# Kernel tuning notes

Hardware: AMD Instinct MI355X
Metric: run time of the kernel (lower is better)

The kernel has to match this reference:

```python
import jax, jax.numpy as jnp
import numpy as np

NB_ATOMS = 1024
NB_CHANNELS = 3
ATOM_SIZE = 16
NONDIFF_STEPS = 30
DIFF_STEPS = 10
TEMP = 100.0
EPS = 1e-8
BATCH = 16384


def setup_inputs() -> dict:
    key = jax.random.key(0)
    k1, k2 = jax.random.split(key)
    y = jax.random.normal(k1, (BATCH, NB_CHANNELS, ATOM_SIZE, ATOM_SIZE), dtype=jnp.float32)
    # init='random': randn / (atom_size * sqrt(nb_channels))
    atoms = jax.random.normal(k2, (NB_ATOMS, NB_CHANNELS, ATOM_SIZE, ATOM_SIZE), dtype=jnp.float32)
    atoms = atoms / (ATOM_SIZE * np.sqrt(NB_CHANNELS).astype(np.float32))
    return {"y": y, "atoms": atoms}


def reference(y, atoms):
    B = y.shape[0]
    A = atoms.shape[0]
    # L1 norms per sample / per atom
    y_norms = jnp.sum(jnp.abs(y.reshape(B, -1)), axis=1).reshape(-1, 1, 1, 1)  # [B,1,1,1]
    a_flat = atoms.reshape(A, -1)
    a_flat = a_flat / jnp.sum(jnp.abs(a_flat), axis=1, keepdims=True)          # [A,D]

    X = a_flat @ a_flat.T                                   # [A,A] gram matrix
    q = a_flat @ (y / y_norms).reshape(B, -1).T             # [A,B]
    coeffs = jnp.full((A, B), 1.0 / A, dtype=y.dtype)

    Xs = jax.lax.stop_gradient(X)
    qs = jax.lax.stop_gradient(q)

    def nondiff_step(i, c):
        grad = Xs @ c - qs                                  # [A,B]
        # faithful to torch: argmin over the BATCH dim, scatter one 1 per atom row
        am = jnp.zeros_like(c).at[jnp.arange(A), jnp.argmin(grad, axis=1)].set(1.0)
        d = am - c
        denom = jnp.sum(d * (Xs @ d)) + EPS                 # scalar (as in torch)
        lam = jnp.clip(-jnp.sum(d * grad, axis=0)[None, :] / denom, 0.0, 1.0)
        return c + d * lam

    coeffs = jax.lax.fori_loop(0, NONDIFF_STEPS, nondiff_step, coeffs)
    coeffs = jax.lax.stop_gradient(coeffs)

    def diff_step(c, _):
        grad = X @ c - q
        sm = jax.nn.softmax(-TEMP * grad, axis=0)           # softmax over atoms
        d = sm - c
        denom = jnp.sum(d * (X @ d)) + EPS
        lam = jnp.clip(-jnp.sum(d * grad, axis=0)[None, :] / denom, 0.0, 1.0)
        return c + d * lam, None

    coeffs, _ = jax.lax.scan(diff_step, coeffs, None, length=DIFF_STEPS)

    # einsum 'ij,ilmn->jlmn' with normalized atoms, rescale by y L1 norms
    recon = (coeffs.T @ a_flat).reshape(B, NB_CHANNELS, ATOM_SIZE, ATOM_SIZE) * y_norms
    return recon
```

## Files before the change

kernel.cpp:

```cpp
#include <hip/hip_runtime.h>
#include <hip/hip_bf16.h>
#include <math.h>

#define A_DIM 1024
#define D_DIM 768
#define B_DIM 16384
#define TEMP_C 100.0f
#define EPS_C 1e-8f


typedef __attribute__((ext_vector_type(8))) short short8;
typedef __attribute__((ext_vector_type(4))) float f32x4;
#define MFMA16(a, b, c) __builtin_amdgcn_mfma_f32_16x16x32_bf16(a, b, c, 0, 0, 0)

typedef __attribute__((address_space(3))) unsigned char lds_byte;
typedef __attribute__((address_space(1))) const unsigned char g_byte;
__device__ __forceinline__ void async_copy16(const void* gptr, void* lptr) {
    __builtin_amdgcn_global_load_lds((g_byte*)gptr, (lds_byte*)lptr, 16, 0, 0);
}

#define SCHED0 __builtin_amdgcn_sched_barrier(0)
#define ASM_BAR asm volatile("s_barrier" ::: "memory")

__device__ __forceinline__ void swz(int i, int& m0, int& n0) {
    int xcd = i & 7, j = i >> 3;
    m0 = ((xcd << 4) + (j >> 3)) << 7;
    n0 = (j & 7) << 7;
}


__device__ __forceinline__ float wave_sum(float v) {
#pragma unroll
    for (int m = 1; m < 64; m <<= 1) v += __shfl_xor(v, m);
    return v;
}
__device__ __forceinline__ float wave_max(float v) {
#pragma unroll
    for (int m = 1; m < 64; m <<= 1) v = fmaxf(v, __shfl_xor(v, m));
    return v;
}

__device__ __forceinline__ float block_reduce_sum(float v, float* red) {
    int t = threadIdx.x;
    v = wave_sum(v);
    if ((t & 63) == 0) red[t >> 6] = v;
    __syncthreads();
    float r = red[0] + red[1] + red[2] + red[3];
    __syncthreads();
    return r;
}

__device__ __forceinline__ float block_reduce_max(float v, float* red) {
    int t = threadIdx.x;
    v = wave_max(v);
    if ((t & 63) == 0) red[t >> 6] = v;
    __syncthreads();
    float r = fmaxf(fmaxf(red[0], red[1]), fmaxf(red[2], red[3]));
    __syncthreads();
    return r;
}

__device__ __forceinline__ void block_reduce_sum3(float& a, float& b, float& c, float* red) {
    int t = threadIdx.x;
    a = wave_sum(a);
    b = wave_sum(b);
    c = wave_sum(c);
    if ((t & 63) == 0) {
        int w = t >> 6;
        red[w] = a; red[4 + w] = b; red[8 + w] = c;
    }
    __syncthreads();
    a = red[0] + red[1] + red[2] + red[3];
    b = red[4] + red[5] + red[6] + red[7];
    c = red[8] + red[9] + red[10] + red[11];
    __syncthreads();
}


__device__ __forceinline__ unsigned int fkey(float v) {
    unsigned int u = __float_as_uint(v);
    return u ^ ((u & 0x80000000u) ? 0xFFFFFFFFu : 0x80000000u);
}

__device__ __forceinline__ unsigned short f2bf(float x) {
    unsigned int u = __float_as_uint(x);
    return (unsigned short)((u + 0x7FFFu + ((u >> 16) & 1u)) >> 16);
}
__device__ __forceinline__ float bf2f(unsigned short h) {
    return __uint_as_float(((unsigned int)h) << 16);
}
__device__ __forceinline__ void split2(float x, unsigned short& hi, unsigned short& lo) {
    hi = f2bf(x);
    lo = f2bf(x - bf2f(hi));
}
__device__ __forceinline__ float clamp01(float x) {
    return fminf(fmaxf(x, 0.f), 1.f);
}


__device__ __forceinline__ void stage_tile8(const unsigned short* gsrc, int stride, int k0,
                                            unsigned short* ltile, int lane) {
    int srow = lane >> 2;
    int scol = (lane & 3) * 8;
#pragma unroll
    for (int s = 0; s < 8; s++) {
        const unsigned short* src = gsrc + (size_t)(s * 16 + srow) * stride + k0 + scol;
        async_copy16(src, ltile + s * 512);
    }
}

__device__ __forceinline__ void mfma_k32(const unsigned short* lds, int wm, int wn, int lane,
                                         f32x4 acc[4][4]) {
    int frow = lane & 15, fk = (lane >> 4) * 8;
    short8 ah[4], al[4], bh[4], bl[4];
#pragma unroll
    for (int t = 0; t < 4; t++) {
        int ar = (wm * 64 + t * 16 + frow) * 32 + fk;
        ah[t] = *(const short8*)&lds[ar];
        al[t] = *(const short8*)&lds[4096 + ar];
        int br = (wn * 64 + t * 16 + frow) * 32 + fk;
        bh[t] = *(const short8*)&lds[8192 + br];
        bl[t] = *(const short8*)&lds[12288 + br];
    }
#pragma unroll
    for (int i = 0; i < 4; i++)
#pragma unroll
        for (int j = 0; j < 4; j++) {
            acc[i][j] = MFMA16(ah[i], bh[j], acc[i][j]);
            acc[i][j] = MFMA16(ah[i], bl[j], acc[i][j]);
            acc[i][j] = MFMA16(al[i], bh[j], acc[i][j]);
        }
}


template <int PART>
__device__ __forceinline__ void stage_part(unsigned short* buf,
                                           const unsigned short* Ahi,
                                           const unsigned short* Alo,
                                           const unsigned short* Xhi,
                                           const unsigned short* Xlo,
                                           int m0, int n0, int k0, int t) {
    constexpr int AHI = 0;
    constexpr int ALO = 8192;
    constexpr int BHI = 16384;
    constexpr int BLO = 24576;
    int r = t >> 2;
    int cg = (t & 3) ^ ((t >> 3) & 3);
    size_t col = (size_t)k0 + cg * 8;
    if constexpr (PART == 0) {
        async_copy16(Ahi + (size_t)(m0 + r) * A_DIM + col,       buf + AHI + t * 8);
        async_copy16(Ahi + (size_t)(m0 + 128 + r) * A_DIM + col, buf + AHI + 4096 + t * 8);
    } else if constexpr (PART == 1) {
        async_copy16(Alo + (size_t)(m0 + r) * A_DIM + col,       buf + ALO + t * 8);
        async_copy16(Alo + (size_t)(m0 + 128 + r) * A_DIM + col, buf + ALO + 4096 + t * 8);
    } else if constexpr (PART == 2) {
        async_copy16(Xhi + (size_t)(n0 + r) * A_DIM + col,       buf + BHI + t * 8);
        async_copy16(Xhi + (size_t)(n0 + 128 + r) * A_DIM + col, buf + BHI + 4096 + t * 8);
    } else {
        async_copy16(Xlo + (size_t)(n0 + r) * A_DIM + col,       buf + BLO + t * 8);
        async_copy16(Xlo + (size_t)(n0 + 128 + r) * A_DIM + col, buf + BLO + 4096 + t * 8);
    }
}

__device__ __forceinline__ void mfma_mi3(short8 ah, short8 al,
                                         const short8 bh[4], const short8 bl[4],
                                         f32x4* accRow) {
#pragma unroll
    for (int j = 0; j < 4; j++) {
        accRow[j] = MFMA16(ah, bh[j], accRow[j]);
        accRow[j] = MFMA16(ah, bl[j], accRow[j]);
        accRow[j] = MFMA16(al, bh[j], accRow[j]);
    }
}

template <int MODE>
__global__ __launch_bounds__(512, 2) void gemm256(const unsigned short* __restrict__ Ahi,
                                                  const unsigned short* __restrict__ Alo,
                                                  const unsigned short* __restrict__ Xhi,
                                                  const unsigned short* __restrict__ Xlo,
                                                  const float* __restrict__ qt,
                                                  unsigned long long* __restrict__ keys,
                                                  float* __restrict__ cxc,
                                                  float* __restrict__ cq,
                                                  float* __restrict__ scal,
                                                  float* __restrict__ G,
                                                  float* __restrict__ scal3,
                                                  float* __restrict__ XC) {
    constexpr int BUFS = 32768;
    constexpr int AHI = 0;
    constexpr int ALO = 8192;
    constexpr int BHI = 16384;
    constexpr int BLO = 24576;
    __shared__ unsigned short lds[2 * BUFS];
    __shared__ float red[8];
    int tid = threadIdx.x;
    if (MODE == 0 && blockIdx.x == 0 && tid < 4) scal[tid] = 0.f;
    int w = tid >> 6, lane = tid & 63;
    int wm = w >> 2, wn = w & 3;
    int bi = blockIdx.x;
    int xcd = bi & 7, bj = bi >> 3;
    int m0 = ((xcd << 3) + (bj >> 2)) << 8;
    int n0 = (bj & 3) << 8;

    f32x4 acc[8][4];
#pragma unroll
    for (int i = 0; i < 8; i++)
#pragma unroll
        for (int j = 0; j < 4; j++) acc[i][j] = f32x4{0.f, 0.f, 0.f, 0.f};

    int frow = lane & 15;
    int sw = ((lane >> 4) ^ ((frow >> 1) & 3)) * 8;

    stage_part<0>(lds, Ahi, Alo, Xhi, Xlo, m0, n0, 0, tid);
    stage_part<1>(lds, Ahi, Alo, Xhi, Xlo, m0, n0, 0, tid);
    stage_part<2>(lds, Ahi, Alo, Xhi, Xlo, m0, n0, 0, tid);
    stage_part<3>(lds, Ahi, Alo, Xhi, Xlo, m0, n0, 0, tid);

    int cur = 0;
    for (int ks = 0; ks < 32; ++ks) {
        unsigned short* rb = lds + cur * BUFS;
        unsigned short* wb = lds + (cur ^ 1) * BUFS;
        const bool pf = (ks < 31);
        const int k1 = (ks + 1) * 32;

        if (pf) {
            stage_part<0>(wb, Ahi, Alo, Xhi, Xlo, m0, n0, k1, tid);
            SCHED0;
            asm volatile("s_waitcnt vmcnt(2)" ::: "memory");
        } else {
            asm volatile("s_waitcnt vmcnt(0)" ::: "memory");
        }
        SCHED0; ASM_BAR; SCHED0;

        short8 bh[4], bl[4];
#pragma unroll
        for (int j = 0; j < 4; j++) {
            int br = wn * 64 + j * 16 + frow;
            bh[j] = *(const short8*)&rb[BHI + br * 32 + sw];
            bl[j] = *(const short8*)&rb[BLO + br * 32 + sw];
        }
        {
            int ar0 = wm * 128 + 0 * 16 + frow, ar1 = wm * 128 + 1 * 16 + frow;
            short8 a0h = *(const short8*)&rb[AHI + ar0 * 32 + sw];
            short8 a1h = *(const short8*)&rb[AHI + ar1 * 32 + sw];
            short8 a0l = *(const short8*)&rb[ALO + ar0 * 32 + sw];
            short8 a1l = *(const short8*)&rb[ALO + ar1 * 32 + sw];
            if (pf) stage_part<1>(wb, Ahi, Alo, Xhi, Xlo, m0, n0, k1, tid);
            SCHED0; ASM_BAR; SCHED0;
            asm volatile("s_waitcnt lgkmcnt(0)" ::: "memory"); SCHED0;
            __builtin_amdgcn_s_setprio(1);
            mfma_mi3(a0h, a0l, bh, bl, acc[0]);
            mfma_mi3(a1h, a1l, bh, bl, acc[1]);
            __builtin_amdgcn_s_setprio(0);
            SCHED0; ASM_BAR; SCHED0;
        }
#pragma unroll
        for (int ph = 1; ph < 4; ph++) {
            int mia = 2 * ph, mib = 2 * ph + 1;
            int ara = wm * 128 + mia * 16 + frow, arb = wm * 128 + mib * 16 + frow;
            short8 aah = *(const short8*)&rb[AHI + ara * 32 + sw];
            short8 abh = *(const short8*)&rb[AHI + arb * 32 + sw];
            short8 aal = *(const short8*)&rb[ALO + ara * 32 + sw];
            short8 abl = *(const short8*)&rb[ALO + arb * 32 + sw];
            if (pf) {
                if (ph == 1) stage_part<2>(wb, Ahi, Alo, Xhi, Xlo, m0, n0, k1, tid);
                if (ph == 2) stage_part<3>(wb, Ahi, Alo, Xhi, Xlo, m0, n0, k1, tid);
            }
            SCHED0; ASM_BAR; SCHED0;
            asm volatile("s_waitcnt lgkmcnt(0)" ::: "memory"); SCHED0;
            __builtin_amdgcn_s_setprio(1);
            mfma_mi3(aah, aal, bh, bl, acc[mia]);
            mfma_mi3(abh, abl, bh, bl, acc[mib]);
            __builtin_amdgcn_s_setprio(0);
            SCHED0; ASM_BAR; SCHED0;
        }
        cur ^= 1;
    }

    int crow = (lane >> 4) * 4, ccol = lane & 15;
    if constexpr (MODE == 0) {
        unsigned long long best[4] = {~0ULL, ~0ULL, ~0ULL, ~0ULL};
#pragma unroll
        for (int mi = 0; mi < 8; mi++)
#pragma unroll
            for (int r = 0; r < 4; r++) {
                int gm = m0 + wm * 128 + mi * 16 + crow + r;
                float pcx = 0.f, pcq = 0.f;
#pragma unroll
                for (int jj = 0; jj < 4; jj++) {
                    int gn = n0 + wn * 64 + jj * 16 + ccol;
                    size_t idx = (size_t)gm * A_DIM + gn;
                    float c = bf2f(Ahi[idx]) + bf2f(Alo[idx]);
                    float q = qt[idx];
                    float xc = acc[mi][jj][r];
                    XC[idx] = xc;
                    pcx += c * xc;
                    pcq += c * q;
                    unsigned long long key =
                        ((unsigned long long)fkey(xc - q) << 32) | (unsigned int)gm;
                    if (key < best[jj]) best[jj] = key;
                }
                for (int mm = 1; mm < 16; mm <<= 1) {
                    pcx += __shfl_xor(pcx, mm, 16);
                    pcq += __shfl_xor(pcq, mm, 16);
                }
                if (ccol == 0) {
                    atomicAdd(&cxc[gm], pcx);
                    atomicAdd(&cq[gm], pcq);
                }
            }
#pragma unroll
        for (int jj = 0; jj < 4; jj++) {
            int gn = n0 + wn * 64 + jj * 16 + ccol;
            unsigned long long o = __shfl_xor(best[jj], 16);
            if (o < best[jj]) best[jj] = o;
            o = __shfl_xor(best[jj], 32);
            if (o < best[jj]) best[jj] = o;
            if ((lane >> 4) == 0) atomicMin(&keys[gn], best[jj]);
        }
    } else {
        float part = 0.f;
#pragma unroll
        for (int mi = 0; mi < 8; mi++)
#pragma unroll
            for (int r = 0; r < 4; r++) {
                int gm = m0 + wm * 128 + mi * 16 + crow + r;
#pragma unroll
                for (int jj = 0; jj < 4; jj++) {
                    int gn = n0 + wn * 64 + jj * 16 + ccol;
                    size_t idx = (size_t)gm * A_DIM + gn;
                    float d = bf2f(Ahi[idx]) + bf2f(Alo[idx]);
                    float xd = acc[mi][jj][r];
                    G[idx] = xd;
                    part += xd * d;
                }
            }
        part = wave_sum(part);
        if (lane == 0) red[w] = part;
        __syncthreads();
        if (tid == 0) {
            float tot = red[0] + red[1] + red[2] + red[3] +
                        red[4] + red[5] + red[6] + red[7];
            atomicAdd(scal3, tot);
        }
    }
}

__global__ __launch_bounds__(512) void fgrad(const float* __restrict__ qt,
                                             unsigned short* __restrict__ Chi,
                                             unsigned short* __restrict__ Clo,
                                             float* __restrict__ XC,
                                             const float* __restrict__ Xf,
                                             const unsigned long long* __restrict__ Kprev,
                                             unsigned long long* __restrict__ Kcur,
                                             float* __restrict__ cxc,
                                             float* __restrict__ cq,
                                             float* __restrict__ num_amg,
                                             const float* __restrict__ scalPrev,
                                             float* __restrict__ scalCur) {
    __shared__ unsigned long long lkeys[8][1024];
    int tid = threadIdx.x;
    if (blockIdx.x == 0 && tid < 4) scalCur[tid] = 0.f;
    int w = tid >> 6, lane = tid & 63;
    int b0 = blockIdx.x * 32;
    float den = scalPrev[0] + scalPrev[1] - 2.f * scalPrev[2] + EPS_C;

    unsigned int klow[16];
#pragma unroll
    for (int s = 0; s < 16; s++) klow[s] = (unsigned int)Kprev[lane + s * 64];

    unsigned long long best[16];
#pragma unroll
    for (int i = 0; i < 16; i++) best[i] = ~0ULL;

    for (int rr = 0; rr < 4; ++rr) {
        int b = b0 + w + rr * 8;
        float lam = clamp01((cxc[b] - cq[b] - num_amg[b]) / den);
        float om = 1.f - lam;
        const bool active = (lam != 0.f);

        unsigned short* hr = Chi + (size_t)b * A_DIM;
        unsigned short* lr = Clo + (size_t)b * A_DIM;
        float* xcr = XC + (size_t)b * A_DIM;
        const float* qr = qt + (size_t)b * A_DIM;
        float dx = 0.f, dq = 0.f;

        if (active) {
            unsigned long long mask[16];
#pragma unroll
            for (int s = 0; s < 16; s++) mask[s] = __ballot(klow[s] == (unsigned int)b);
#pragma unroll
            for (int ch = 0; ch < 4; ++ch) {
                int col = ch * 256 + lane * 4;
                ushort4 hv = *(const ushort4*)(hr + col);
                ushort4 lv = *(const ushort4*)(lr + col);
                float4 xv = *(const float4*)(xcr + col);
                float4 qv = *(const float4*)(qr + col);
                int sel = lane >> 4;
                unsigned long long mw =
                    (sel == 0) ? mask[ch * 4 + 0] :
                    (sel == 1) ? mask[ch * 4 + 1] :
                    (sel == 2) ? mask[ch * 4 + 2] : mask[ch * 4 + 3];
                unsigned int ind4 = (unsigned int)((mw >> ((lane & 15) * 4)) & 0xFULL);
                float c0 = om * (bf2f(hv.x) + bf2f(lv.x)) + ((ind4 & 1u) ? lam : 0.f);
                float c1 = om * (bf2f(hv.y) + bf2f(lv.y)) + ((ind4 & 2u) ? lam : 0.f);
                float c2 = om * (bf2f(hv.z) + bf2f(lv.z)) + ((ind4 & 4u) ? lam : 0.f);
                float c3 = om * (bf2f(hv.w) + bf2f(lv.w)) + ((ind4 & 8u) ? lam : 0.f);
                xv.x *= om; xv.y *= om; xv.z *= om; xv.w *= om;
#pragma unroll
                for (int s = 0; s < 16; s++) {
                    unsigned long long m = mask[s];
                    while (m) {
                        int a = __ffsll(m) - 1 + s * 64;
                        m &= m - 1;
                        float4 av = *(const float4*)(Xf + (size_t)a * A_DIM + col);
                        xv.x += lam * av.x; xv.y += lam * av.y;
                        xv.z += lam * av.z; xv.w += lam * av.w;
                    }
                }
                split2(c0, hv.x, lv.x);
                split2(c1, hv.y, lv.y);
                split2(c2, hv.z, lv.z);
                split2(c3, hv.w, lv.w);
                *(ushort4*)(hr + col) = hv;
                *(ushort4*)(lr + col) = lv;
                *(float4*)(xcr + col) = xv;
                float g0 = xv.x - qv.x, g1 = xv.y - qv.y, g2 = xv.z - qv.z, g3 = xv.w - qv.w;
                dx += c0 * xv.x + c1 * xv.y + c2 * xv.z + c3 * xv.w;
                dq += c0 * qv.x + c1 * qv.y + c2 * qv.z + c3 * qv.w;
                unsigned long long k0 = ((unsigned long long)fkey(g0) << 32) | (unsigned int)b;
                unsigned long long k1 = ((unsigned long long)fkey(g1) << 32) | (unsigned int)b;
                unsigned long long k2 = ((unsigned long long)fkey(g2) << 32) | (unsigned int)b;
                unsigned long long k3 = ((unsigned long long)fkey(g3) << 32) | (unsigned int)b;
                if (k0 < best[ch * 4 + 0]) best[ch * 4 + 0] = k0;
                if (k1 < best[ch * 4 + 1]) best[ch * 4 + 1] = k1;
                if (k2 < best[ch * 4 + 2]) best[ch * 4 + 2] = k2;
                if (k3 < best[ch * 4 + 3]) best[ch * 4 + 3] = k3;
            }
        } else {
#pragma unroll
            for (int ch = 0; ch < 4; ++ch) {
                int col = ch * 256 + lane * 4;
                ushort4 hv = *(const ushort4*)(hr + col);
                ushort4 lv = *(const ushort4*)(lr + col);
                float4 xv = *(const float4*)(xcr + col);
                float4 qv = *(const float4*)(qr + col);
                float c0 = bf2f(hv.x) + bf2f(lv.x);
                float c1 = bf2f(hv.y) + bf2f(lv.y);
                float c2 = bf2f(hv.z) + bf2f(lv.z);
                float c3 = bf2f(hv.w) + bf2f(lv.w);
                float g0 = xv.x - qv.x, g1 = xv.y - qv.y, g2 = xv.z - qv.z, g3 = xv.w - qv.w;
                dx += c0 * xv.x + c1 * xv.y + c2 * xv.z + c3 * xv.w;
                dq += c0 * qv.x + c1 * qv.y + c2 * qv.z + c3 * qv.w;
                unsigned long long k0 = ((unsigned long long)fkey(g0) << 32) | (unsigned int)b;
                unsigned long long k1 = ((unsigned long long)fkey(g1) << 32) | (unsigned int)b;
                unsigned long long k2 = ((unsigned long long)fkey(g2) << 32) | (unsigned int)b;
                unsigned long long k3 = ((unsigned long long)fkey(g3) << 32) | (unsigned int)b;
                if (k0 < best[ch * 4 + 0]) best[ch * 4 + 0] = k0;
                if (k1 < best[ch * 4 + 1]) best[ch * 4 + 1] = k1;
                if (k2 < best[ch * 4 + 2]) best[ch * 4 + 2] = k2;
                if (k3 < best[ch * 4 + 3]) best[ch * 4 + 3] = k3;
            }
        }
        dx = wave_sum(dx);
        dq = wave_sum(dq);
        if (lane == 0) {
            cxc[b] = dx;
            cq[b] = dq;
            num_amg[b] = 0.f;
        }
    }
#pragma unroll
    for (int ch = 0; ch < 4; ++ch)
#pragma unroll
        for (int j = 0; j < 4; ++j)
            lkeys[w][ch * 256 + lane * 4 + j] = best[ch * 4 + j];
    __syncthreads();
    for (int i = tid; i < 1024; i += 512) {
        unsigned long long v = lkeys[0][i];
        if (lkeys[1][i] < v) v = lkeys[1][i];
        if (lkeys[2][i] < v) v = lkeys[2][i];
        if (lkeys[3][i] < v) v = lkeys[3][i];
        if (lkeys[4][i] < v) v = lkeys[4][i];
        if (lkeys[5][i] < v) v = lkeys[5][i];
        if (lkeys[6][i] < v) v = lkeys[6][i];
        if (lkeys[7][i] < v) v = lkeys[7][i];
        atomicMin(&Kcur[i], v);
    }
}


__global__ __launch_bounds__(256) void ynorm_split_kernel(const float* __restrict__ y,
                                                          float* __restrict__ ynorm,
                                                          unsigned short* __restrict__ Ynh,
                                                          unsigned short* __restrict__ Ynl) {
    __shared__ float red[16];
    int b = blockIdx.x;
    const float* row = y + (size_t)b * D_DIM;
    float s = 0.f;
    for (int i = threadIdx.x; i < D_DIM; i += 256) s += fabsf(row[i]);
    float tot = block_reduce_sum(s, red);
    float inv = 1.f / tot;
    unsigned short* oh = Ynh + (size_t)b * D_DIM;
    unsigned short* ol = Ynl + (size_t)b * D_DIM;
    for (int i = threadIdx.x; i < D_DIM; i += 256) {
        unsigned short h, l;
        split2(row[i] * inv, h, l);
        oh[i] = h; ol[i] = l;
    }
    if (threadIdx.x == 0) ynorm[b] = tot;
}

__global__ __launch_bounds__(256) void anorm_kernel(const float* __restrict__ atoms,
                                                    float* __restrict__ an,
                                                    float* __restrict__ anrm,
                                                    unsigned short* __restrict__ Anh,
                                                    unsigned short* __restrict__ Anl) {
    __shared__ float red[16];
    int a = blockIdx.x;
    const float* row = atoms + (size_t)a * D_DIM;
    float s = 0.f;
    for (int i = threadIdx.x; i < D_DIM; i += 256) s += fabsf(row[i]);
    float tot = block_reduce_sum(s, red);
    float inv = 1.f / tot;
    for (int i = threadIdx.x; i < D_DIM; i += 256) {
        float v = row[i] * inv;
        an[(size_t)a * D_DIM + i] = v;
        unsigned short h, l;
        split2(v, h, l);
        Anh[(size_t)a * D_DIM + i] = h;
        Anl[(size_t)a * D_DIM + i] = l;
    }
    if (threadIdx.x == 0) anrm[a] = tot;
}

__global__ __launch_bounds__(256) void atrans_split_kernel(const float* __restrict__ atoms,
                                                           const float* __restrict__ anrm,
                                                           unsigned short* __restrict__ AnTh,
                                                           unsigned short* __restrict__ AnTl) {
    int n = blockIdx.x;
    for (int k = threadIdx.x; k < A_DIM; k += 256) {
        float v = atoms[(size_t)k * D_DIM + n] / anrm[k];
        unsigned short h, l;
        split2(v, h, l);
        AnTh[(size_t)n * A_DIM + k] = h;
        AnTl[(size_t)n * A_DIM + k] = l;
    }
}

__global__ __launch_bounds__(256) void split_kernel(const float* __restrict__ src,
                                                    unsigned short* __restrict__ hi,
                                                    unsigned short* __restrict__ lo,
                                                    int n4) {
    int i = blockIdx.x * 256 + threadIdx.x;
    if (i < n4) {
        float4 v = ((const float4*)src)[i];
        ushort4 h, l;
        split2(v.x, h.x, l.x);
        split2(v.y, h.y, l.y);
        split2(v.z, h.z, l.z);
        split2(v.w, h.w, l.w);
        ((ushort4*)hi)[i] = h;
        ((ushort4*)lo)[i] = l;
    }
}

__global__ __launch_bounds__(256) void fill_pair_kernel(unsigned short* __restrict__ Chi,
                                                        unsigned short* __restrict__ Clo,
                                                        size_t n4) {
    size_t i = (size_t)blockIdx.x * 256 + threadIdx.x;
    if (i < n4) {
        unsigned short h, l;
        split2(1.f / A_DIM, h, l);
        ((ushort4*)Chi)[i] = make_ushort4(h, h, h, h);
        ((ushort4*)Clo)[i] = make_ushort4(l, l, l, l);
    }
}

__global__ __launch_bounds__(256) void gemm_xt(const float* __restrict__ Aop,
                                               float* __restrict__ Cout) {
    const int LDT = 132;
    const int N = A_DIM, K = D_DIM;
    __shared__ float As[16 * LDT];
    __shared__ float Bs[16 * LDT];
    int m0 = blockIdx.y * 128, n0 = blockIdx.x * 128;
    int tid = threadIdx.x;
    int tx = tid & 15, ty = tid >> 4;
    float acc[8][8];
#pragma unroll
    for (int i = 0; i < 8; i++)
#pragma unroll
        for (int j = 0; j < 8; j++) acc[i][j] = 0.f;
    for (int k0 = 0; k0 < K; k0 += 16) {
#pragma unroll
        for (int s = 0; s < 2; s++) {
            int idx = tid + s * 256;
            int row = idx >> 2, kq = (idx & 3) * 4;
            float4 v = *(const float4*)(Aop + (size_t)(m0 + row) * K + k0 + kq);
            As[(kq + 0) * LDT + row] = v.x;
            As[(kq + 1) * LDT + row] = v.y;
            As[(kq + 2) * LDT + row] = v.z;
            As[(kq + 3) * LDT + row] = v.w;
        }
#pragma unroll
        for (int s = 0; s < 2; s++) {
            int idx = tid + s * 256;
            int row = idx >> 2, kq = (idx & 3) * 4;
            float4 v = *(const float4*)(Aop + (size_t)(n0 + row) * K + k0 + kq);
            Bs[(kq + 0) * LDT + row] = v.x;
            Bs[(kq + 1) * LDT + row] = v.y;
            Bs[(kq + 2) * LDT + row] = v.z;
            Bs[(kq + 3) * LDT + row] = v.w;
        }
        __syncthreads();
#pragma unroll
        for (int kk = 0; kk < 16; kk++) {
            float a[8], b[8];
            *(float4*)(a)     = *(const float4*)(As + kk * LDT + ty * 8);
            *(float4*)(a + 4) = *(const float4*)(As + kk * LDT + ty * 8 + 4);
            *(float4*)(b)     = *(const float4*)(Bs + kk * LDT + tx * 8);
            *(float4*)(b + 4) = *(const float4*)(Bs + kk * LDT + tx * 8 + 4);
#pragma unroll
            for (int i = 0; i < 8; i++)
#pragma unroll
                for (int j = 0; j < 8; j++) acc[i][j] = fmaf(a[i], b[j], acc[i][j]);
        }
        __syncthreads();
    }
#pragma unroll
    for (int i = 0; i < 8; i++) {
        int row = m0 + ty * 8 + i;
#pragma unroll
        for (int j = 0; j < 8; j += 4) {
            int col = n0 + tx * 8 + j;
            float4 v = make_float4(acc[i][j], acc[i][j + 1], acc[i][j + 2], acc[i][j + 3]);
            *(float4*)(Cout + (size_t)row * N + col) = v;
        }
    }
}

__global__ __launch_bounds__(256) void qt_mfma(const unsigned short* __restrict__ Ynh,
                                               const unsigned short* __restrict__ Ynl,
                                               const unsigned short* __restrict__ Anh,
                                               const unsigned short* __restrict__ Anl,
                                               float* __restrict__ qt) {
    __shared__ unsigned short lds[16384];
    int tid = threadIdx.x;
    int w = tid >> 6, lane = tid & 63;
    int wm = w >> 1, wn = w & 1;
    int m0, n0;
    swz(blockIdx.x, m0, n0);

    f32x4 acc[4][4];
#pragma unroll
    for (int i = 0; i < 4; i++)
#pragma unroll
        for (int j = 0; j < 4; j++) acc[i][j] = f32x4{0.f, 0.f, 0.f, 0.f};

    const unsigned short* gsrc;
    if (w == 0) gsrc = Ynh + (size_t)m0 * D_DIM;
    else if (w == 1) gsrc = Ynl + (size_t)m0 * D_DIM;
    else if (w == 2) gsrc = Anh + (size_t)n0 * D_DIM;
    else gsrc = Anl + (size_t)n0 * D_DIM;
    unsigned short* ltile = lds + w * 4096;
    for (int k0 = 0; k0 < D_DIM; k0 += 32) {
        stage_tile8(gsrc, D_DIM, k0, ltile, lane);
        __syncthreads();
        mfma_k32(lds, wm, wn, lane, acc);
        __syncthreads();
    }

    int crow = (lane >> 4) * 4, ccol = lane & 15;
#pragma unroll
    for (int i = 0; i < 4; i++) {
        int gm = m0 + wm * 64 + i * 16 + crow;
#pragma unroll
        for (int j = 0; j < 4; j++) {
            int gn = n0 + wn * 64 + j * 16 + ccol;
#pragma unroll
            for (int r = 0; r < 4; r++)
                qt[(size_t)(gm + r) * A_DIM + gn] = acc[i][j][r];
        }
    }
}


__global__ __launch_bounds__(256) void init_kernel(unsigned long long* __restrict__ keys,
                                                   float* __restrict__ num_amg,
                                                   float* __restrict__ cxc,
                                                   float* __restrict__ cq,
                                                   float* __restrict__ scal) {
    int i = blockIdx.x * 256 + threadIdx.x;
    num_amg[i] = 0.f;
    cxc[i] = 0.f;
    cq[i] = 0.f;
    if (i < 2 * A_DIM) keys[i] = ~0ULL;
    if (i < 8) scal[i] = 0.f;
}

__global__ __launch_bounds__(256) void stats_kernel(const float* __restrict__ Xf,
                                                    const unsigned long long* __restrict__ Kcur,
                                                    const unsigned short* __restrict__ Chi,
                                                    const unsigned short* __restrict__ Clo,
                                                    const float* __restrict__ qt,
                                                    const float* __restrict__ cxc,
                                                    float* __restrict__ num_amg,
                                                    float* __restrict__ scalCur,
                                                    unsigned long long* __restrict__ Knext) {
    __shared__ float red[16];
    int a = blockIdx.x;
    int ba = (int)(unsigned int)(Kcur[a] & 0xFFFFFFFFULL);
    const float* xr = Xf + (size_t)a * A_DIM;
    const unsigned short* ch = Chi + (size_t)ba * A_DIM;
    const unsigned short* cl = Clo + (size_t)ba * A_DIM;
    float ps = 0.f, xs = 0.f;
    for (int i = threadIdx.x; i < A_DIM; i += 256) {
        float xv = xr[i];
        if ((int)(unsigned int)(Kcur[i] & 0xFFFFFFFFULL) == ba) ps += xv;
        xs += xv * (bf2f(ch[i]) + bf2f(cl[i]));
    }
    float s1p = (threadIdx.x < 16) ? cxc[(a << 4) + threadIdx.x] : 0.f;
    block_reduce_sum3(ps, xs, s1p, red);
    if (threadIdx.x == 0) {
        atomicAdd(&scalCur[0], ps);
        atomicAdd(&scalCur[2], xs);
        atomicAdd(&scalCur[1], s1p);
        atomicAdd(&num_amg[ba], xs - qt[(size_t)ba * A_DIM + a]);
        Knext[a] = ~0ULL;
    }
}

__global__ __launch_bounds__(256) void ndupdate_c(unsigned short* __restrict__ Chi,
                                                  unsigned short* __restrict__ Clo,
                                                  const unsigned long long* __restrict__ Kprev,
                                                  float* __restrict__ cxc,
                                                  float* __restrict__ cq,
                                                  float* __restrict__ num_amg,
                                                  const float* __restrict__ scalPrev) {
    int b = blockIdx.x;
    float den = scalPrev[0] + scalPrev[1] - 2.f * scalPrev[2] + EPS_C;
    float lam = clamp01((cxc[b] - cq[b] - num_amg[b]) / den);
    float om = 1.f - lam;
    int i = threadIdx.x;
    ushort4* h4 = (ushort4*)(Chi + (size_t)b * A_DIM);
    ushort4* l4 = (ushort4*)(Clo + (size_t)b * A_DIM);
    ushort4 h = h4[i], l = l4[i];
    int b0 = (int)(unsigned int)Kprev[i * 4 + 0];
    int b1 = (int)(unsigned int)Kprev[i * 4 + 1];
    int b2 = (int)(unsigned int)Kprev[i * 4 + 2];
    int b3 = (int)(unsigned int)Kprev[i * 4 + 3];
    float c0 = om * (bf2f(h.x) + bf2f(l.x)) + ((b0 == b) ? lam : 0.f);
    float c1 = om * (bf2f(h.y) + bf2f(l.y)) + ((b1 == b) ? lam : 0.f);
    float c2 = om * (bf2f(h.z) + bf2f(l.z)) + ((b2 == b) ? lam : 0.f);
    float c3 = om * (bf2f(h.w) + bf2f(l.w)) + ((b3 == b) ? lam : 0.f);
    split2(c0, h.x, l.x);
    split2(c1, h.y, l.y);
    split2(c2, h.z, l.z);
    split2(c3, h.w, l.w);
    h4[i] = h; l4[i] = l;
    __syncthreads();
    if (i == 0) {
        cxc[b] = 0.f;
        cq[b] = 0.f;
        num_amg[b] = 0.f;
    }
}

__global__ __launch_bounds__(256) void ndupdate_full(unsigned short* __restrict__ Chi,
                                                     unsigned short* __restrict__ Clo,
                                                     const unsigned long long* __restrict__ Kprev,
                                                     const float* __restrict__ cxc,
                                                     const float* __restrict__ cq,
                                                     const float* __restrict__ num_amg,
                                                     const float* __restrict__ scalPrev,
                                                     float* __restrict__ XC,
                                                     const float* __restrict__ Xf) {
    __shared__ int mlist[1024];
    __shared__ int mcount;
    int b = blockIdx.x;
    int i = threadIdx.x;
    if (i == 0) mcount = 0;
    float den = scalPrev[0] + scalPrev[1] - 2.f * scalPrev[2] + EPS_C;
    float lam = clamp01((cxc[b] - cq[b] - num_amg[b]) / den);
    float om = 1.f - lam;
    ushort4* h4 = (ushort4*)(Chi + (size_t)b * A_DIM);
    ushort4* l4 = (ushort4*)(Clo + (size_t)b * A_DIM);
    ushort4 h = h4[i], l = l4[i];
    int b0 = (int)(unsigned int)Kprev[i * 4 + 0];
    int b1 = (int)(unsigned int)Kprev[i * 4 + 1];
    int b2 = (int)(unsigned int)Kprev[i * 4 + 2];
    int b3 = (int)(unsigned int)Kprev[i * 4 + 3];
    float c0 = om * (bf2f(h.x) + bf2f(l.x)) + ((b0 == b) ? lam : 0.f);
    float c1 = om * (bf2f(h.y) + bf2f(l.y)) + ((b1 == b) ? lam : 0.f);
    float c2 = om * (bf2f(h.z) + bf2f(l.z)) + ((b2 == b) ? lam : 0.f);
    float c3 = om * (bf2f(h.w) + bf2f(l.w)) + ((b3 == b) ? lam : 0.f);
    split2(c0, h.x, l.x);
    split2(c1, h.y, l.y);
    split2(c2, h.z, l.z);
    split2(c3, h.w, l.w);
    h4[i] = h; l4[i] = l;
    __syncthreads();
    for (int a = i; a < A_DIM; a += 256)
        if ((int)(unsigned int)Kprev[a] == b) { int p = atomicAdd(&mcount, 1); mlist[p] = a; }
    __syncthreads();
    float4 xv = *(float4*)(XC + (size_t)b * A_DIM + i * 4);
    xv.x *= om; xv.y *= om; xv.z *= om; xv.w *= om;
    int mc = mcount;
    for (int m = 0; m < mc; m++) {
        float4 av = *(const float4*)(Xf + (size_t)mlist[m] * A_DIM + i * 4);
        xv.x += lam * av.x; xv.y += lam * av.y;
        xv.z += lam * av.z; xv.w += lam * av.w;
    }
    *(float4*)(XC + (size_t)b * A_DIM + i * 4) = xv;
}


__global__ __launch_bounds__(256) void rinit_kernel(float* __restrict__ XC,
                                                    const float* __restrict__ qt) {
    size_t i = (size_t)blockIdx.x * 256 + threadIdx.x;
    float4 x = ((const float4*)XC)[i];
    float4 q = ((const float4*)qt)[i];
    x.x -= q.x; x.y -= q.y; x.z -= q.z; x.w -= q.w;
    ((float4*)XC)[i] = x;
}

__global__ __launch_bounds__(256) void softmax_kernel(const float* __restrict__ R,
                                                      unsigned short* __restrict__ Chi,
                                                      unsigned short* __restrict__ Clo,
                                                      float* __restrict__ num_cg,
                                                      float* __restrict__ scal3) {
    __shared__ float red[16];
    int b = blockIdx.x;
    int i = threadIdx.x;
    if (b == 0 && i == 0) *scal3 = 0.f;
    const float4* g4 = (const float4*)(R + (size_t)b * A_DIM);
    ushort4* h4 = (ushort4*)(Chi + (size_t)b * A_DIM);
    ushort4* l4 = (ushort4*)(Clo + (size_t)b * A_DIM);
    float4 g = g4[i];
    ushort4 h = h4[i], l = l4[i];
    float c0 = bf2f(h.x) + bf2f(l.x);
    float c1 = bf2f(h.y) + bf2f(l.y);
    float c2 = bf2f(h.z) + bf2f(l.z);
    float c3 = bf2f(h.w) + bf2f(l.w);
    float4 t = make_float4(-TEMP_C * g.x, -TEMP_C * g.y, -TEMP_C * g.z, -TEMP_C * g.w);
    float m = fmaxf(fmaxf(t.x, t.y), fmaxf(t.z, t.w));
    float M = block_reduce_max(m, red);
    float4 e = make_float4(expf(t.x - M), expf(t.y - M), expf(t.z - M), expf(t.w - M));
    float S = block_reduce_sum(e.x + e.y + e.z + e.w, red);
    float inv = 1.f / S;
    float4 sm = make_float4(e.x * inv, e.y * inv, e.z * inv, e.w * inv);
    float np = (c0 - sm.x) * g.x + (c1 - sm.y) * g.y + (c2 - sm.z) * g.z + (c3 - sm.w) * g.w;
    split2(sm.x - c0, h.x, l.x);
    split2(sm.y - c1, h.y, l.y);
    split2(sm.z - c2, h.z, l.z);
    split2(sm.w - c3, h.w, l.w);
    h4[i] = h; l4[i] = l;
    float nt = block_reduce_sum(np, red);
    if (i == 0) num_cg[b] = nt;
}

template <int LAST>
__global__ __launch_bounds__(256) void dupdate_fused(float* __restrict__ R,
                                                     const float* __restrict__ Xd,
                                                     unsigned short* __restrict__ Chi,
                                                     unsigned short* __restrict__ Clo,
                                                     float* __restrict__ num_cg,
                                                     const float* __restrict__ s3cur,
                                                     float* __restrict__ s3next) {
    __shared__ float red[16];
    int b = blockIdx.x;
    int i = threadIdx.x;
    if (!LAST && b == 0 && i == 0) *s3next = 0.f;
    float4* r4 = (float4*)(R + (size_t)b * A_DIM);
    float4 g = r4[i];
    float4 t = make_float4(-TEMP_C * g.x, -TEMP_C * g.y, -TEMP_C * g.z, -TEMP_C * g.w);
    float m = fmaxf(fmaxf(t.x, t.y), fmaxf(t.z, t.w));
    float M = block_reduce_max(m, red);
    float4 e = make_float4(expf(t.x - M), expf(t.y - M), expf(t.z - M), expf(t.w - M));
    float S = block_reduce_sum(e.x + e.y + e.z + e.w, red);
    float inv = 1.f / S;
    float4 sm = make_float4(e.x * inv, e.y * inv, e.z * inv, e.w * inv);
    float den = *s3cur + EPS_C;
    float lam = clamp01(num_cg[b] / den);
    float om = 1.f - lam;
    ushort4* h4 = (ushort4*)(Chi + (size_t)b * A_DIM);
    ushort4* l4 = (ushort4*)(Clo + (size_t)b * A_DIM);
    ushort4 h = h4[i], l = l4[i];
    float c0 = sm.x - om * (bf2f(h.x) + bf2f(l.x));
    float c1 = sm.y - om * (bf2f(h.y) + bf2f(l.y));
    float c2 = sm.z - om * (bf2f(h.z) + bf2f(l.z));
    float c3 = sm.w - om * (bf2f(h.w) + bf2f(l.w));
    float4 xd = ((const float4*)(Xd + (size_t)b * A_DIM))[i];
    g.x += lam * xd.x; g.y += lam * xd.y;
    g.z += lam * xd.z; g.w += lam * xd.w;
    r4[i] = g;
    if (LAST) {
        split2(c0, h.x, l.x);
        split2(c1, h.y, l.y);
        split2(c2, h.z, l.z);
        split2(c3, h.w, l.w);
        h4[i] = h; l4[i] = l;
    } else {
        float4 t2 = make_float4(-TEMP_C * g.x, -TEMP_C * g.y, -TEMP_C * g.z, -TEMP_C * g.w);
        float m2 = fmaxf(fmaxf(t2.x, t2.y), fmaxf(t2.z, t2.w));
        float M2 = block_reduce_max(m2, red);
        float4 e2 = make_float4(expf(t2.x - M2), expf(t2.y - M2),
                                expf(t2.z - M2), expf(t2.w - M2));
        float S2 = block_reduce_sum(e2.x + e2.y + e2.z + e2.w, red);
        float inv2 = 1.f / S2;
        float4 sm2 = make_float4(e2.x * inv2, e2.y * inv2, e2.z * inv2, e2.w * inv2);
        float np = (c0 - sm2.x) * g.x + (c1 - sm2.y) * g.y +
                   (c2 - sm2.z) * g.z + (c3 - sm2.w) * g.w;
        split2(sm2.x - c0, h.x, l.x);
        split2(sm2.y - c1, h.y, l.y);
        split2(sm2.z - c2, h.z, l.z);
        split2(sm2.w - c3, h.w, l.w);
        h4[i] = h; l4[i] = l;
        float nt = block_reduce_sum(np, red);
        if (i == 0) num_cg[b] = nt;
    }
}

__global__ __launch_bounds__(256) void mfma_recon(const unsigned short* __restrict__ Chi,
                                                  const unsigned short* __restrict__ Clo,
                                                  const unsigned short* __restrict__ AnTh,
                                                  const unsigned short* __restrict__ AnTl,
                                                  const float* __restrict__ ynorm,
                                                  float* __restrict__ out) {
    __shared__ unsigned short lds[16384];
    int tid = threadIdx.x;
    int w = tid >> 6, lane = tid & 63;
    int wm = w >> 1, wn = w & 1;
    int m0 = blockIdx.y * 128, n0 = blockIdx.x * 128;

    f32x4 acc[4][4];
#pragma unroll
    for (int i = 0; i < 4; i++)
#pragma unroll
        for (int j = 0; j < 4; j++) acc[i][j] = f32x4{0.f, 0.f, 0.f, 0.f};

    const unsigned short* gsrc;
    if (w == 0) gsrc = Chi + (size_t)m0 * A_DIM;
    else if (w == 1) gsrc = Clo + (size_t)m0 * A_DIM;
    else if (w == 2) gsrc = AnTh + (size_t)n0 * A_DIM;
    else gsrc = AnTl + (size_t)n0 * A_DIM;
    unsigned short* ltile = lds + w * 4096;
    for (int k0 = 0; k0 < A_DIM; k0 += 32) {
        stage_tile8(gsrc, A_DIM, k0, ltile, lane);
        __syncthreads();
        mfma_k32(lds, wm, wn, lane, acc);
        __syncthreads();
    }

    int crow = (lane >> 4) * 4, ccol = lane & 15;
#pragma unroll
    for (int i = 0; i < 4; i++) {
        int gm = m0 + wm * 64 + i * 16 + crow;
#pragma unroll
        for (int j = 0; j < 4; j++) {
            int gn = n0 + wn * 64 + j * 16 + ccol;
#pragma unroll
            for (int r = 0; r < 4; r++)
                out[(size_t)(gm + r) * D_DIM + gn] = acc[i][j][r] * ynorm[gm + r];
        }
    }
}


extern "C" void kernel_launch(void* const* d_in, const int* in_sizes, int n_in,
                              void* d_out, int out_size, void* d_ws, size_t ws_size,
                              hipStream_t stream) {
    const float* y = (const float*)d_in[0];
    const float* atoms = (const float*)d_in[1];
    float* out = (float*)d_out;

    char* ws = (char*)d_ws;
    size_t off = 0;
    auto alloc = [&](size_t bytes) -> void* {
        void* p = ws + off;
        off += (bytes + 255) & ~(size_t)255;
        return p;
    };
    const size_t BA = (size_t)B_DIM * A_DIM;
    unsigned short* Chi = (unsigned short*)alloc(BA * 2);
    unsigned short* Clo = (unsigned short*)alloc(BA * 2);
    float* Greg = (float*)alloc(BA * 4);
    float* qt = (float*)alloc(BA * 4);
    unsigned short* Xhi = (unsigned short*)alloc((size_t)A_DIM * A_DIM * 2);
    unsigned short* Xlo = (unsigned short*)alloc((size_t)A_DIM * A_DIM * 2);
    float* Xf = (float*)alloc((size_t)A_DIM * A_DIM * 4);
    float* ynorm = (float*)alloc(B_DIM * 4);
    float* anrm  = (float*)alloc(A_DIM * 4);
    float* cxc   = (float*)alloc(B_DIM * 4);
    float* cq    = (float*)alloc(B_DIM * 4);
    float* num_amg = (float*)alloc(B_DIM * 4);
    float* num_cg  = (float*)alloc(B_DIM * 4);
    unsigned long long* keys = (unsigned long long*)alloc(2 * A_DIM * 8);
    float* scal = (float*)alloc(256);
    (void)ws_size; (void)in_sizes; (void)n_in; (void)out_size;

    float* an = Greg;
    unsigned short* Anh = (unsigned short*)(an + (size_t)A_DIM * D_DIM);
    unsigned short* Anl = Anh + (size_t)A_DIM * D_DIM;
    unsigned short* Ynh = Anl + (size_t)A_DIM * D_DIM;
    unsigned short* Ynl = Ynh + (size_t)B_DIM * D_DIM;
    float* XC = Greg;
    float* R  = Greg;
    float* Xd = qt;
    unsigned short* AnTh = (unsigned short*)Greg;
    unsigned short* AnTl = (unsigned short*)Greg + (size_t)D_DIM * A_DIM;

    ynorm_split_kernel<<<B_DIM, 256, 0, stream>>>(y, ynorm, Ynh, Ynl);
    anorm_kernel<<<A_DIM, 256, 0, stream>>>(atoms, an, anrm, Anh, Anl);
    gemm_xt<<<dim3(A_DIM / 128, A_DIM / 128), 256, 0, stream>>>(an, Xf);
    split_kernel<<<A_DIM * A_DIM / 4 / 256, 256, 0, stream>>>(Xf, Xhi, Xlo, A_DIM * A_DIM / 4);
    qt_mfma<<<1024, 256, 0, stream>>>(Ynh, Ynl, Anh, Anl, qt);
    fill_pair_kernel<<<(int)(BA / 4 / 256), 256, 0, stream>>>(Chi, Clo, BA / 4);
    init_kernel<<<B_DIM / 256, 256, 0, stream>>>(keys, num_amg, cxc, cq, scal);

    for (int t = 0; t < 30; t++) {
        int cur = t & 1, prev = 1 - cur;
        unsigned long long* Kcur = keys + cur * A_DIM;
        unsigned long long* Kprev = keys + prev * A_DIM;
        unsigned long long* Knext = keys + ((t + 1) & 1) * A_DIM;
        float* sCur = scal + cur * 4;
        float* sPrev = scal + prev * 4;
        if ((t & 7) == 0) {
            gemm256<0><<<256, 512, 0, stream>>>(Chi, Clo, Xhi, Xlo, qt,
                                                Kcur, cxc, cq, scal, nullptr, nullptr, XC);
        } else {
            fgrad<<<512, 512, 0, stream>>>(qt, Chi, Clo, XC, Xf, Kprev, Kcur,
                                           cxc, cq, num_amg, sPrev, sCur);
        }
        stats_kernel<<<A_DIM, 256, 0, stream>>>(Xf, Kcur, Chi, Clo, qt, cxc,
                                                num_amg, sCur, Knext);
        if (t == 7 || t == 15 || t == 23)
            ndupdate_c<<<B_DIM, 256, 0, stream>>>(Chi, Clo, Kcur, cxc, cq,
                                                  num_amg, sCur);
        if (t == 29)
            ndupdate_full<<<B_DIM, 256, 0, stream>>>(Chi, Clo, Kcur, cxc, cq,
                                                     num_amg, sCur, XC, Xf);
    }

    rinit_kernel<<<(int)(BA / 4 / 256), 256, 0, stream>>>(XC, qt);
    softmax_kernel<<<B_DIM, 256, 0, stream>>>(R, Chi, Clo, num_cg, &scal[3]);
    for (int t = 0; t < 10; t++) {
        float* s3cur = &scal[3 + (t & 1) * 4];
        float* s3next = &scal[3 + ((t + 1) & 1) * 4];
        gemm256<3><<<256, 512, 0, stream>>>(Chi, Clo, Xhi, Xlo, nullptr,
                                            nullptr, nullptr, nullptr, nullptr,
                                            Xd, s3cur, nullptr);
        if (t < 9)
            dupdate_fused<0><<<B_DIM, 256, 0, stream>>>(R, Xd, Chi, Clo, num_cg,
                                                        s3cur, s3next);
        else
            dupdate_fused<1><<<B_DIM, 256, 0, stream>>>(R, Xd, Chi, Clo, num_cg,
                                                        s3cur, nullptr);
    }

    atrans_split_kernel<<<D_DIM, 256, 0, stream>>>(atoms, anrm, AnTh, AnTl);
    mfma_recon<<<dim3(D_DIM / 128, B_DIM / 128), 256, 0, stream>>>(Chi, Clo, AnTh, AnTl,
                                                                   ynorm, out);
}
```

Measured before the change: 5.369 ms.

## Carry gradient G instead of X·C, drop rinit, refresh with GEMM less often

The nondiff loop now stores the gradient G = XC - q directly and updates it incrementally (G = om*G + lam*X[a] - lam*q). cq is tracked as a scalar recurrence, and cxc is recovered as cg + cq, so fgrad no longer reads q in the inactive path. This removes the separate rinit pass before the softmax. Full GEMM recomputes drop from every 8 steps to steps 0 and 16, with matching ndupdate_c calls, which saves two large GEMMs. In exchange, more incremental fp32 updates run between refreshes, so drift against the exact product can grow.

```diff
diff --git a/kernel.cpp b/kernel.cpp
--- a/kernel.cpp
+++ b/kernel.cpp
@@ -185,7 +185,7 @@
                                                   float* __restrict__ scal,
                                                   float* __restrict__ G,
                                                   float* __restrict__ scal3,
-                                                  float* __restrict__ XC) {
+                                                  float* __restrict__ Gout) {
     constexpr int BUFS = 32768;
     constexpr int AHI = 0;
     constexpr int ALO = 8192;
@@ -293,11 +293,12 @@
                     float c = bf2f(Ahi[idx]) + bf2f(Alo[idx]);
                     float q = qt[idx];
                     float xc = acc[mi][jj][r];
-                    XC[idx] = xc;
+                    float g = xc - q;
+                    Gout[idx] = g;
                     pcx += c * xc;
                     pcq += c * q;
                     unsigned long long key =
-                        ((unsigned long long)fkey(xc - q) << 32) | (unsigned int)gm;
+                        ((unsigned long long)fkey(g) << 32) | (unsigned int)gm;
                     if (key < best[jj]) best[jj] = key;
                 }
                 for (int mm = 1; mm < 16; mm <<= 1) {
@@ -349,7 +350,7 @@
 __global__ __launch_bounds__(512) void fgrad(const float* __restrict__ qt,
                                              unsigned short* __restrict__ Chi,
                                              unsigned short* __restrict__ Clo,
-                                             float* __restrict__ XC,
+                                             float* __restrict__ G,
                                              const float* __restrict__ Xf,
                                              const unsigned long long* __restrict__ Kprev,
                                              unsigned long long* __restrict__ Kcur,
@@ -375,15 +376,16 @@
 
     for (int rr = 0; rr < 4; ++rr) {
         int b = b0 + w + rr * 8;
-        float lam = clamp01((cxc[b] - cq[b] - num_amg[b]) / den);
+        float cqold = cq[b];
+        float lam = clamp01((cxc[b] - cqold - num_amg[b]) / den);
         float om = 1.f - lam;
         const bool active = (lam != 0.f);
 
         unsigned short* hr = Chi + (size_t)b * A_DIM;
         unsigned short* lr = Clo + (size_t)b * A_DIM;
-        float* xcr = XC + (size_t)b * A_DIM;
+        float* gr = G + (size_t)b * A_DIM;
         const float* qr = qt + (size_t)b * A_DIM;
-        float dx = 0.f, dq = 0.f;
+        float cg = 0.f, sq = 0.f;
 
         if (active) {
             unsigned long long mask[16];
@@ -394,7 +396,7 @@
                 int col = ch * 256 + lane * 4;
                 ushort4 hv = *(const ushort4*)(hr + col);
                 ushort4 lv = *(const ushort4*)(lr + col);
-                float4 xv = *(const float4*)(xcr + col);
+                float4 gv = *(const float4*)(gr + col);
                 float4 qv = *(const float4*)(qr + col);
                 int sel = lane >> 4;
                 unsigned long long mw =
@@ -406,7 +408,7 @@
                 float c1 = om * (bf2f(hv.y) + bf2f(lv.y)) + ((ind4 & 2u) ? lam : 0.f);
                 float c2 = om * (bf2f(hv.z) + bf2f(lv.z)) + ((ind4 & 4u) ? lam : 0.f);
                 float c3 = om * (bf2f(hv.w) + bf2f(lv.w)) + ((ind4 & 8u) ? lam : 0.f);
-                xv.x *= om; xv.y *= om; xv.z *= om; xv.w *= om;
+                gv.x *= om; gv.y *= om; gv.z *= om; gv.w *= om;
 #pragma unroll
                 for (int s = 0; s < 16; s++) {
                     unsigned long long m = mask[s];
@@ -414,24 +416,26 @@
                         int a = __ffsll(m) - 1 + s * 64;
                         m &= m - 1;
                         float4 av = *(const float4*)(Xf + (size_t)a * A_DIM + col);
-                        xv.x += lam * av.x; xv.y += lam * av.y;
-                        xv.z += lam * av.z; xv.w += lam * av.w;
+                        gv.x += lam * av.x; gv.y += lam * av.y;
+                        gv.z += lam * av.z; gv.w += lam * av.w;
                     }
                 }
+                gv.x -= lam * qv.x; gv.y -= lam * qv.y;
+                gv.z -= lam * qv.z; gv.w -= lam * qv.w;
+                sq += ((ind4 & 1u) ? qv.x : 0.f) + ((ind4 & 2u) ? qv.y : 0.f) +
+                      ((ind4 & 4u) ? qv.z : 0.f) + ((ind4 & 8u) ? qv.w : 0.f);
                 split2(c0, hv.x, lv.x);
                 split2(c1, hv.y, lv.y);
                 split2(c2, hv.z, lv.z);
                 split2(c3, hv.w, lv.w);
                 *(ushort4*)(hr + col) = hv;
                 *(ushort4*)(lr + col) = lv;
-                *(float4*)(xcr + col) = xv;
-                float g0 = xv.x - qv.x, g1 = xv.y - qv.y, g2 = xv.z - qv.z, g3 = xv.w - qv.w;
-                dx += c0 * xv.x + c1 * xv.y + c2 * xv.z + c3 * xv.w;
-                dq += c0 * qv.x + c1 * qv.y + c2 * qv.z + c3 * qv.w;
-                unsigned long long k0 = ((unsigned long long)fkey(g0) << 32) | (unsigned int)b;
-                unsigned long long k1 = ((unsigned long long)fkey(g1) << 32) | (unsigned int)b;
-                unsigned long long k2 = ((unsigned long long)fkey(g2) << 32) | (unsigned int)b;
-                unsigned long long k3 = ((unsigned long long)fkey(g3) << 32) | (unsigned int)b;
+                *(float4*)(gr + col) = gv;
+                cg += c0 * gv.x + c1 * gv.y + c2 * gv.z + c3 * gv.w;
+                unsigned long long k0 = ((unsigned long long)fkey(gv.x) << 32) | (unsigned int)b;
+                unsigned long long k1 = ((unsigned long long)fkey(gv.y) << 32) | (unsigned int)b;
+                unsigned long long k2 = ((unsigned long long)fkey(gv.z) << 32) | (unsigned int)b;
+                unsigned long long k3 = ((unsigned long long)fkey(gv.w) << 32) | (unsigned int)b;
                 if (k0 < best[ch * 4 + 0]) best[ch * 4 + 0] = k0;
                 if (k1 < best[ch * 4 + 1]) best[ch * 4 + 1] = k1;
                 if (k2 < best[ch * 4 + 2]) best[ch * 4 + 2] = k2;
@@ -443,30 +447,28 @@
                 int col = ch * 256 + lane * 4;
                 ushort4 hv = *(const ushort4*)(hr + col);
                 ushort4 lv = *(const ushort4*)(lr + col);
-                float4 xv = *(const float4*)(xcr + col);
-                float4 qv = *(const float4*)(qr + col);
+                float4 gv = *(const float4*)(gr + col);
                 float c0 = bf2f(hv.x) + bf2f(lv.x);
                 float c1 = bf2f(hv.y) + bf2f(lv.y);
                 float c2 = bf2f(hv.z) + bf2f(lv.z);
                 float c3 = bf2f(hv.w) + bf2f(lv.w);
-                float g0 = xv.x - qv.x, g1 = xv.y - qv.y, g2 = xv.z - qv.z, g3 = xv.w - qv.w;
-                dx += c0 * xv.x + c1 * xv.y + c2 * xv.z + c3 * xv.w;
-                dq += c0 * qv.x + c1 * qv.y + c2 * qv.z + c3 * qv.w;
-                unsigned long long k0 = ((unsigned long long)fkey(g0) << 32) | (unsigned int)b;
-                unsigned long long k1 = ((unsigned long long)fkey(g1) << 32) | (unsigned int)b;
-                unsigned long long k2 = ((unsigned long long)fkey(g2) << 32) | (unsigned int)b;
-                unsigned long long k3 = ((unsigned long long)fkey(g3) << 32) | (unsigned int)b;
+                cg += c0 * gv.x + c1 * gv.y + c2 * gv.z + c3 * gv.w;
+                unsigned long long k0 = ((unsigned long long)fkey(gv.x) << 32) | (unsigned int)b;
+                unsigned long long k1 = ((unsigned long long)fkey(gv.y) << 32) | (unsigned int)b;
+                unsigned long long k2 = ((unsigned long long)fkey(gv.z) << 32) | (unsigned int)b;
+                unsigned long long k3 = ((unsigned long long)fkey(gv.w) << 32) | (unsigned int)b;
                 if (k0 < best[ch * 4 + 0]) best[ch * 4 + 0] = k0;
                 if (k1 < best[ch * 4 + 1]) best[ch * 4 + 1] = k1;
                 if (k2 < best[ch * 4 + 2]) best[ch * 4 + 2] = k2;
                 if (k3 < best[ch * 4 + 3]) best[ch * 4 + 3] = k3;
             }
         }
-        dx = wave_sum(dx);
-        dq = wave_sum(dq);
+        cg = wave_sum(cg);
+        if (active) sq = wave_sum(sq);
         if (lane == 0) {
-            cxc[b] = dx;
-            cq[b] = dq;
+            float cqn = active ? (om * cqold + lam * sq) : cqold;
+            cq[b] = cqn;
+            cxc[b] = cg + cqn;
             num_amg[b] = 0.f;
         }
     }
@@ -773,8 +775,9 @@
                                                      const float* __restrict__ cq,
                                                      const float* __restrict__ num_amg,
                                                      const float* __restrict__ scalPrev,
-                                                     float* __restrict__ XC,
-                                                     const float* __restrict__ Xf) {
+                                                     float* __restrict__ G,
+                                                     const float* __restrict__ Xf,
+                                                     const float* __restrict__ qt) {
     __shared__ int mlist[1024];
     __shared__ int mcount;
     int b = blockIdx.x;
@@ -803,26 +806,20 @@
     for (int a = i; a < A_DIM; a += 256)
         if ((int)(unsigned int)Kprev[a] == b) { int p = atomicAdd(&mcount, 1); mlist[p] = a; }
     __syncthreads();
-    float4 xv = *(float4*)(XC + (size_t)b * A_DIM + i * 4);
-    xv.x *= om; xv.y *= om; xv.z *= om; xv.w *= om;
+    float4 gv = *(float4*)(G + (size_t)b * A_DIM + i * 4);
+    float4 qv = *(const float4*)(qt + (size_t)b * A_DIM + i * 4);
+    gv.x *= om; gv.y *= om; gv.z *= om; gv.w *= om;
     int mc = mcount;
     for (int m = 0; m < mc; m++) {
         float4 av = *(const float4*)(Xf + (size_t)mlist[m] * A_DIM + i * 4);
-        xv.x += lam * av.x; xv.y += lam * av.y;
-        xv.z += lam * av.z; xv.w += lam * av.w;
-    }
-    *(float4*)(XC + (size_t)b * A_DIM + i * 4) = xv;
-}
-
-
-__global__ __launch_bounds__(256) void rinit_kernel(float* __restrict__ XC,
-                                                    const float* __restrict__ qt) {
-    size_t i = (size_t)blockIdx.x * 256 + threadIdx.x;
-    float4 x = ((const float4*)XC)[i];
-    float4 q = ((const float4*)qt)[i];
-    x.x -= q.x; x.y -= q.y; x.z -= q.z; x.w -= q.w;
-    ((float4*)XC)[i] = x;
-}
+        gv.x += lam * av.x; gv.y += lam * av.y;
+        gv.z += lam * av.z; gv.w += lam * av.w;
+    }
+    gv.x -= lam * qv.x; gv.y -= lam * qv.y;
+    gv.z -= lam * qv.z; gv.w -= lam * qv.w;
+    *(float4*)(G + (size_t)b * A_DIM + i * 4) = gv;
+}
+
 
 __global__ __launch_bounds__(256) void softmax_kernel(const float* __restrict__ R,
                                                       unsigned short* __restrict__ Chi,
@@ -1004,8 +1001,7 @@
     unsigned short* Anl = Anh + (size_t)A_DIM * D_DIM;
     unsigned short* Ynh = Anl + (size_t)A_DIM * D_DIM;
     unsigned short* Ynl = Ynh + (size_t)B_DIM * D_DIM;
-    float* XC = Greg;
-    float* R  = Greg;
+    float* G = Greg;
     float* Xd = qt;
     unsigned short* AnTh = (unsigned short*)Greg;
     unsigned short* AnTl = (unsigned short*)Greg + (size_t)D_DIM * A_DIM;
@@ -1025,25 +1021,24 @@
         unsigned long long* Knext = keys + ((t + 1) & 1) * A_DIM;
         float* sCur = scal + cur * 4;
         float* sPrev = scal + prev * 4;
-        if ((t & 7) == 0) {
+        if (t == 0 || t == 16) {
             gemm256<0><<<256, 512, 0, stream>>>(Chi, Clo, Xhi, Xlo, qt,
-                                                Kcur, cxc, cq, scal, nullptr, nullptr, XC);
+                                                Kcur, cxc, cq, scal, nullptr, nullptr, G);
         } else {
-            fgrad<<<512, 512, 0, stream>>>(qt, Chi, Clo, XC, Xf, Kprev, Kcur,
+            fgrad<<<512, 512, 0, stream>>>(qt, Chi, Clo, G, Xf, Kprev, Kcur,
                                            cxc, cq, num_amg, sPrev, sCur);
         }
         stats_kernel<<<A_DIM, 256, 0, stream>>>(Xf, Kcur, Chi, Clo, qt, cxc,
                                                 num_amg, sCur, Knext);
-        if (t == 7 || t == 15 || t == 23)
+        if (t == 15)
             ndupdate_c<<<B_DIM, 256, 0, stream>>>(Chi, Clo, Kcur, cxc, cq,
                                                   num_amg, sCur);
         if (t == 29)
             ndupdate_full<<<B_DIM, 256, 0, stream>>>(Chi, Clo, Kcur, cxc, cq,
-                                                     num_amg, sCur, XC, Xf);
-    }
-
-    rinit_kernel<<<(int)(BA / 4 / 256), 256, 0, stream>>>(XC, qt);
-    softmax_kernel<<<B_DIM, 256, 0, stream>>>(R, Chi, Clo, num_cg, &scal[3]);
+                                                     num_amg, sCur, G, Xf, qt);
+    }
+
+    softmax_kernel<<<B_DIM, 256, 0, stream>>>(G, Chi, Clo, num_cg, &scal[3]);
     for (int t = 0; t < 10; t++) {
         float* s3cur = &scal[3 + (t & 1) * 4];
         float* s3next = &scal[3 + ((t + 1) & 1) * 4];
@@ -1051,10 +1046,10 @@
                                             nullptr, nullptr, nullptr, nullptr,
                                             Xd, s3cur, nullptr);
         if (t < 9)
-            dupdate_fused<0><<<B_DIM, 256, 0, stream>>>(R, Xd, Chi, Clo, num_cg,
+            dupdate_fused<0><<<B_DIM, 256, 0, stream>>>(G, Xd, Chi, Clo, num_cg,
                                                         s3cur, s3next);
         else
-            dupdate_fused<1><<<B_DIM, 256, 0, stream>>>(R, Xd, Chi, Clo, num_cg,
+            dupdate_fused<1><<<B_DIM, 256, 0, stream>>>(G, Xd, Chi, Clo, num_cg,
                                                         s3cur, nullptr);
     }
 
```

After: 5.030 ms. 6.3% less time.
